# Performance work log

Hardware: AMD Instinct MI355X
Metric: run time of the kernel (lower is better)

## Reference

```python
import jax, jax.numpy as jnp
import numpy as np

B, S, E, H = 256, 512, 128, 256


def setup_inputs() -> dict:
    key = jax.random.key(0)
    ks = jax.random.split(key, 20)
    s = lambda *sh: 1.0 / np.sqrt(sh[-1])
    inp = jax.random.uniform(ks[0], (B, S, 2), dtype=jnp.float32)
    W_emb = jax.random.normal(ks[1], (E, 2), jnp.float32) * 0.5
    dec_input = jax.random.normal(ks[2], (E,), jnp.float32) * 0.1
    # encoder LSTM (input E -> hidden H), pytorch gate order i,f,g,o
    enc_Wih = jax.random.normal(ks[3], (4 * H, E), jnp.float32) * s(E)
    enc_Whh = jax.random.normal(ks[4], (4 * H, H), jnp.float32) * s(H)
    enc_bih = jnp.zeros((4 * H,), jnp.float32)
    enc_bhh = jnp.zeros((4 * H,), jnp.float32)
    # process block LSTM (input E -> hidden H)
    pb_Wih = jax.random.normal(ks[5], (4 * H, E), jnp.float32) * s(E)
    pb_Whh = jax.random.normal(ks[6], (4 * H, H), jnp.float32) * s(H)
    pb_bih = jnp.zeros((4 * H,), jnp.float32)
    pb_bhh = jnp.zeros((4 * H,), jnp.float32)
    # attention: W_q Linear(H,H), W_ref Conv1d(H,H,1), v vector
    Wq = jax.random.normal(ks[7], (H, H), jnp.float32) * s(H)
    bq = jnp.zeros((H,), jnp.float32)
    Wref = jax.random.normal(ks[8], (H, H), jnp.float32) * s(H)
    bref = jnp.zeros((H,), jnp.float32)
    V = jax.random.normal(ks[9], (H,), jnp.float32) * s(H)
    # decoder: Linear(H,H,bias=False) -> ReLU -> Linear(H,1,bias=False)
    Wd1 = jax.random.normal(ks[10], (H, H), jnp.float32) * s(H)
    Wd2 = jax.random.normal(ks[11], (1, H), jnp.float32) * s(H)
    return dict(inp=inp, W_emb=W_emb, dec_input=dec_input,
                enc_Wih=enc_Wih, enc_Whh=enc_Whh, enc_bih=enc_bih, enc_bhh=enc_bhh,
                pb_Wih=pb_Wih, pb_Whh=pb_Whh, pb_bih=pb_bih, pb_bhh=pb_bhh,
                Wq=Wq, bq=bq, Wref=Wref, bref=bref, V=V, Wd1=Wd1, Wd2=Wd2)


def _lstm_step(Whh):
    def step(carry, x_proj):
        h, c = carry
        g = x_proj + h @ Whh.T  # [B,4H]
        i, f, gg, o = jnp.split(g, 4, axis=-1)
        c = jax.nn.sigmoid(f) * c + jax.nn.sigmoid(i) * jnp.tanh(gg)
        h = jax.nn.sigmoid(o) * jnp.tanh(c)
        return (h, c), h
    return step


def reference(inp, W_emb, dec_input,
              enc_Wih, enc_Whh, enc_bih, enc_bhh,
              pb_Wih, pb_Whh, pb_bih, pb_bhh,
              Wq, bq, Wref, bref, V, Wd1, Wd2):
    b, seq, _ = inp.shape
    hdim = enc_Whh.shape[1]
    emb = inp @ W_emb.T  # [B,S,E]

    # ---- encoder LSTM over the sequence ----
    x_proj = emb @ enc_Wih.T + enc_bih + enc_bhh  # [B,S,4H]
    h0 = jnp.zeros((b, hdim), inp.dtype)
    c0 = jnp.zeros((b, hdim), inp.dtype)
    (h, c), hs = jax.lax.scan(_lstm_step(enc_Whh), (h0, c0),
                              jnp.swapaxes(x_proj, 0, 1))
    enc_out = jnp.swapaxes(hs, 0, 1)  # [B,S,H]

    # ---- process block: seq steps of single-step LSTM with constant input ----
    xp = dec_input @ pb_Wih.T + pb_bih + pb_bhh  # [4H]
    xp = jnp.broadcast_to(xp, (b, xp.shape[0]))
    step = _lstm_step(pb_Whh)
    (h, c), _ = jax.lax.scan(lambda carry, _: (step(carry, xp)[0], None),
                             (h, c), None, length=seq)

    # ---- attention (glimpse) with final hidden; inner iter loop is idempotent ----
    ref = enc_out @ Wref.T + bref            # [B,S,H]  (Conv1d kernel=1)
    q = h @ Wq.T + bq                        # [B,H]
    u = jnp.tanh(ref + q[:, None, :]) @ V    # [B,S]
    align = jax.nn.softmax(u, axis=-1)
    g_l = jnp.einsum('bs,bsh->bh', align, enc_out)  # glimpse [B,H]

    # ---- decoder head ----
    out = (jax.nn.relu(g_l @ Wd1.T)) @ Wd2.T  # [B,1]
    return out.squeeze(-1)
```

## Files before the change

kernel.cpp:

```cpp
#include <hip/hip_runtime.h>

#define B_ 256
#define S_ 512
#define E_ 128
#define H_ 256
#define FH_ 1024
#define HROW 264

typedef __bf16 bf16x8 __attribute__((ext_vector_type(8)));
typedef float f32x4 __attribute__((ext_vector_type(4)));
typedef unsigned short u16x4 __attribute__((ext_vector_type(4)));
typedef unsigned short u16x8 __attribute__((ext_vector_type(8)));

__device__ __forceinline__ unsigned short f2bf(float f) {
  union { float f; unsigned int u; } a; a.f = f;
  unsigned int u = a.u;
  u += 0x7fffu + ((u >> 16) & 1u);
  return (unsigned short)(u >> 16);
}
__device__ __forceinline__ float bf2f(unsigned short v) {
  union { unsigned int u; float f; } a; a.u = ((unsigned int)v) << 16;
  return a.f;
}
__device__ __forceinline__ float sigm(float x) { return 1.f / (1.f + __expf(-x)); }
__device__ __forceinline__ float tanh_(float x) {
  float e = __expf(2.f * x);
  return 1.f - 2.f / (e + 1.f);
}

#define OFF_ENC    ((size_t)0)
#define OFF_WHHE   ((size_t)67108864)
#define OFF_WHHP   ((size_t)67633152)
#define OFF_WREF   ((size_t)68157440)
#define OFF_MENC   ((size_t)68288512)
#define OFF_BIASE  ((size_t)68296704)
#define OFF_XPV    ((size_t)68300800)
#define OFF_FLAGS  ((size_t)68304896)
#define OFF_HX     ((size_t)68305920)
#define OFF_HFIN   ((size_t)68568064)
#define OFF_QBUF   ((size_t)68830208)
#define OFF_UBUF   ((size_t)69092352)

__global__ void k0_prep(const float* __restrict__ eWih, const float* __restrict__ eWhh,
                        const float* __restrict__ ebih, const float* __restrict__ ebhh,
                        const float* __restrict__ pWih, const float* __restrict__ pWhh,
                        const float* __restrict__ pbih, const float* __restrict__ pbhh,
                        const float* __restrict__ W_emb, const float* __restrict__ dec_in,
                        const float* __restrict__ Wref,
                        unsigned short* __restrict__ WhhE, unsigned short* __restrict__ WhhP,
                        unsigned short* __restrict__ Wrefb,
                        float* __restrict__ Menc, float* __restrict__ biasE,
                        float* __restrict__ xpv,
                        unsigned int* __restrict__ flags, float* __restrict__ ubuf) {
  int gid = blockIdx.x * blockDim.x + threadIdx.x;
  int NT = gridDim.x * blockDim.x;
  for (int i = gid; i < FH_ * H_; i += NT) {
    WhhE[i] = f2bf(eWhh[i]);
    WhhP[i] = f2bf(pWhh[i]);
  }
  for (int i = gid; i < H_ * H_; i += NT) Wrefb[i] = f2bf(Wref[i]);
  for (int i = gid; i < B_ * S_; i += NT) ubuf[i] = 0.f;
  if (gid < 256) flags[gid] = 0u;
  if (gid < FH_) {
    int n = gid;
    float m0 = 0.f, m1 = 0.f, xs = 0.f;
    for (int e = 0; e < E_; ++e) {
      float w = eWih[n * E_ + e];
      m0 += w * W_emb[e * 2 + 0];
      m1 += w * W_emb[e * 2 + 1];
      xs += pWih[n * E_ + e] * dec_in[e];
    }
    Menc[n * 2 + 0] = m0;
    Menc[n * 2 + 1] = m1;
    biasE[n] = ebih[n] + ebhh[n];
    xpv[n] = xs + pbih[n] + pbhh[n];
  }
}

__launch_bounds__(512)
__attribute__((amdgpu_waves_per_eu(2, 2)))
__global__ void k1_lstm(const float* __restrict__ inp,
                        const unsigned short* __restrict__ WhhE,
                        const unsigned short* __restrict__ WhhP,
                        const float* __restrict__ Menc, const float* __restrict__ biasE,
                        const float* __restrict__ xpv,
                        unsigned short* __restrict__ enc_out,
                        unsigned short* __restrict__ hx,
                        unsigned int* __restrict__ flags,
                        float* __restrict__ hfin) {
  __shared__ unsigned short hbuf[16 * HROW];
  __shared__ float xin[16][2];
  const int tid = threadIdx.x;
  const int wave = tid >> 6, lane = tid & 63, quad = lane >> 4, l16 = lane & 15;
  const int blk = blockIdx.x;
  const int grp = (blk & 7) | ((blk >> 4) << 3);
  const int half = (blk >> 3) & 1;
  const int kloc = (wave << 4) | l16;
  const int kcol = half * 128 + kloc;

  for (int i = tid; i < 16 * HROW; i += 512) hbuf[i] = 0;
  if (tid < 32) xin[tid >> 1][tid & 1] = inp[((grp * 16 + (tid >> 1)) * S_ + 0) * 2 + (tid & 1)];

  float c[4] = {0.f, 0.f, 0.f, 0.f};
  float hreg[4] = {0.f, 0.f, 0.f, 0.f};
  f32x4 W00, W01, W02, W03, W04, W05, W06, W07;
  f32x4 W10, W11, W12, W13, W14, W15, W16, W17;
  f32x4 W20, W21, W22, W23, W24, W25, W26, W27;
  f32x4 W30, W31, W32, W33, W34, W35, W36, W37;
  float m0c[4], m1c[4], bc[4];
  unsigned int* myflag = flags + grp * 2 + half;
  unsigned int* pflag = flags + grp * 2 + (1 - half);
  const f32x4 z4 = {0.f, 0.f, 0.f, 0.f};
  __syncthreads();

  int t = 0;
#pragma unroll 1
  for (int phase = 0; phase < 2; ++phase) {
    const unsigned short* W = phase ? WhhP : WhhE;
#define WLOAD(g)                                                        \
    {                                                                   \
      const unsigned short* wp = W + (g * 256 + kcol) * H_ + quad * 8;  \
      W##g##0 = *(const f32x4*)(wp + 0 * 32);                           \
      W##g##1 = *(const f32x4*)(wp + 1 * 32);                           \
      W##g##2 = *(const f32x4*)(wp + 2 * 32);                           \
      W##g##3 = *(const f32x4*)(wp + 3 * 32);                           \
      W##g##4 = *(const f32x4*)(wp + 4 * 32);                           \
      W##g##5 = *(const f32x4*)(wp + 5 * 32);                           \
      W##g##6 = *(const f32x4*)(wp + 6 * 32);                           \
      W##g##7 = *(const f32x4*)(wp + 7 * 32);                           \
    }
    WLOAD(0) WLOAD(1) WLOAD(2) WLOAD(3)
#undef WLOAD
    asm volatile(""
                 : "+v"(W00), "+v"(W01), "+v"(W02), "+v"(W03),
                   "+v"(W04), "+v"(W05), "+v"(W06), "+v"(W07),
                   "+v"(W10), "+v"(W11), "+v"(W12), "+v"(W13),
                   "+v"(W14), "+v"(W15), "+v"(W16), "+v"(W17),
                   "+v"(W20), "+v"(W21), "+v"(W22), "+v"(W23),
                   "+v"(W24), "+v"(W25), "+v"(W26), "+v"(W27),
                   "+v"(W30), "+v"(W31), "+v"(W32), "+v"(W33),
                   "+v"(W34), "+v"(W35), "+v"(W36), "+v"(W37));
#pragma unroll
    for (int gg = 0; gg < 4; ++gg) {
      int n = gg * 256 + kcol;
      if (phase == 0) {
        m0c[gg] = Menc[n * 2 + 0]; m1c[gg] = Menc[n * 2 + 1]; bc[gg] = biasE[n];
      } else {
        m0c[gg] = 0.f; m1c[gg] = 0.f; bc[gg] = xpv[n];
      }
    }
#pragma unroll 1
    for (int step = 0; step < 512; ++step, ++t) {
      float xpre = 0.f;
      if (phase == 0 && tid < 32) {
        int sN = (step < 511) ? step + 1 : 511;
        xpre = inp[((grp * 16 + (tid >> 1)) * S_ + sN) * 2 + (tid & 1)];
      }
      f32x4 acc0 = z4, acc1 = z4, acc2 = z4, acc3 = z4;
#define MSTEP(kt)                                                              \
      {                                                                        \
        bf16x8 Af = *(const bf16x8*)(hbuf + l16 * HROW + kt * 32 + quad * 8);  \
        acc0 = __builtin_amdgcn_mfma_f32_16x16x32_bf16(                        \
            Af, __builtin_bit_cast(bf16x8, W0##kt), acc0, 0, 0, 0);            \
        acc1 = __builtin_amdgcn_mfma_f32_16x16x32_bf16(                        \
            Af, __builtin_bit_cast(bf16x8, W1##kt), acc1, 0, 0, 0);            \
        acc2 = __builtin_amdgcn_mfma_f32_16x16x32_bf16(                        \
            Af, __builtin_bit_cast(bf16x8, W2##kt), acc2, 0, 0, 0);            \
        acc3 = __builtin_amdgcn_mfma_f32_16x16x32_bf16(                        \
            Af, __builtin_bit_cast(bf16x8, W3##kt), acc3, 0, 0, 0);            \
      }
      MSTEP(0) MSTEP(1) MSTEP(2) MSTEP(3) MSTEP(4) MSTEP(5) MSTEP(6) MSTEP(7)
#undef MSTEP
      unsigned short hb[4];
#pragma unroll
      for (int r = 0; r < 4; ++r) {
        int bl = quad * 4 + r;
        float x0 = xin[bl][0], x1 = xin[bl][1];
        float gi = acc0[r] + x0 * m0c[0] + x1 * m1c[0] + bc[0];
        float gf = acc1[r] + x0 * m0c[1] + x1 * m1c[1] + bc[1];
        float gc = acc2[r] + x0 * m0c[2] + x1 * m1c[2] + bc[2];
        float go = acc3[r] + x0 * m0c[3] + x1 * m1c[3] + bc[3];
        float cn = sigm(gf) * c[r] + sigm(gi) * tanh_(gc);
        c[r] = cn;
        hreg[r] = sigm(go) * tanh_(cn);
        hb[r] = f2bf(hreg[r]);
      }
      if (phase == 0) {
#pragma unroll
        for (int r = 0; r < 4; ++r)
          enc_out[(((size_t)(grp * 16 + quad * 4 + r) * S_ + step)) * H_ + kcol] = hb[r];
      }
      {
        unsigned short* hxs = hx + ((size_t)((t & 1) * 32 + grp * 2 + half)) * 2048;
        unsigned long long pack = (unsigned long long)hb[0] |
                                  ((unsigned long long)hb[1] << 16) |
                                  ((unsigned long long)hb[2] << 32) |
                                  ((unsigned long long)hb[3] << 48);
        __hip_atomic_store((unsigned long long*)(hxs + kloc * 16 + quad * 4), pack,
                           __ATOMIC_RELAXED, __HIP_MEMORY_SCOPE_AGENT);
      }
      __syncthreads();
      if (phase == 0 && tid < 32) xin[tid >> 1][tid & 1] = xpre;
      if (tid == 0) {
        __hip_atomic_store(myflag, (unsigned int)(t + 1), __ATOMIC_RELAXED,
                           __HIP_MEMORY_SCOPE_AGENT);
        while (__hip_atomic_load(pflag, __ATOMIC_RELAXED, __HIP_MEMORY_SCOPE_AGENT) <
               (unsigned int)(t + 1)) {
          __builtin_amdgcn_s_sleep(1);
        }
      }
      __syncthreads();
#pragma unroll
      for (int r = 0; r < 4; ++r) hbuf[(quad * 4 + r) * HROW + kcol] = hb[r];
      {
        const unsigned short* ph = hx + ((size_t)((t & 1) * 32 + grp * 2 + (1 - half))) * 2048;
        unsigned long long pv = __hip_atomic_load(
            (const unsigned long long*)(ph + tid * 4), __ATOMIC_RELAXED,
            __HIP_MEMORY_SCOPE_AGENT);
        int kp = tid >> 2, r0 = (tid & 3) * 4;
        unsigned short* dst = hbuf + (1 - half) * 128 + kp;
        dst[(size_t)(r0 + 0) * HROW] = (unsigned short)(pv);
        dst[(size_t)(r0 + 1) * HROW] = (unsigned short)(pv >> 16);
        dst[(size_t)(r0 + 2) * HROW] = (unsigned short)(pv >> 32);
        dst[(size_t)(r0 + 3) * HROW] = (unsigned short)(pv >> 48);
      }
      __syncthreads();
    }
  }
#pragma unroll
  for (int r = 0; r < 4; ++r)
    hfin[(grp * 16 + quad * 4 + r) * H_ + kcol] = hreg[r];
}

__global__ void k1b_q(const float* __restrict__ hfin, const float* __restrict__ Wq,
                      const float* __restrict__ bq, float* __restrict__ qbuf) {
  __shared__ float hl[H_];
  int b = blockIdx.x, j = threadIdx.x;
  hl[j] = hfin[b * H_ + j];
  __syncthreads();
  float s = bq[j];
  const float* w = Wq + j * H_;
  for (int k = 0; k < H_; ++k) s += hl[k] * w[k];
  qbuf[b * H_ + j] = s;
}

__launch_bounds__(512)
__global__ void k2_att(const unsigned short* __restrict__ enc_out,
                       const unsigned short* __restrict__ Wrefb,
                       const float* __restrict__ qbuf, const float* __restrict__ bref,
                       const float* __restrict__ V, float* __restrict__ ubuf) {
  __shared__ unsigned short Bs[128 * HROW];
  __shared__ float qs[128], Vs[128];
  int tid = threadIdx.x;
  int wave = tid >> 6, lane = tid & 63, quad = lane >> 4, l16 = lane & 15;
  int rowblk = blockIdx.x >> 1, nb = blockIdx.x & 1;
  int b = rowblk >> 2;
  {
    int nl = tid >> 2, seg = tid & 3;
    const unsigned short* src = Wrefb + (nb * 128 + nl) * H_ + seg * 64;
    unsigned short* dst = Bs + nl * HROW + seg * 64;
#pragma unroll
    for (int i = 0; i < 8; ++i) *(u16x8*)(dst + i * 8) = *(const u16x8*)(src + i * 8);
  }
  if (tid < 128) {
    int j = nb * 128 + tid;
    qs[tid] = qbuf[b * H_ + j] + bref[j];
    Vs[tid] = V[j];
  }
  __syncthreads();
  int rw = rowblk * 128 + wave * 16 + l16;
  const f32x4 z4 = {0.f, 0.f, 0.f, 0.f};
  f32x4 acc[8];
#pragma unroll
  for (int kt = 0; kt < 8; ++kt) {
    bf16x8 af = *(const bf16x8*)(enc_out + (size_t)rw * H_ + kt * 32 + quad * 8);
#pragma unroll
    for (int nt = 0; nt < 8; ++nt) {
      bf16x8 bfr = *(const bf16x8*)(Bs + (nt * 16 + l16) * HROW + kt * 32 + quad * 8);
      acc[nt] = __builtin_amdgcn_mfma_f32_16x16x32_bf16(af, bfr, (kt == 0) ? z4 : acc[nt],
                                                        0, 0, 0);
    }
  }
  float part[4] = {0.f, 0.f, 0.f, 0.f};
#pragma unroll
  for (int nt = 0; nt < 8; ++nt) {
    float qv = qs[nt * 16 + l16], vv = Vs[nt * 16 + l16];
#pragma unroll
    for (int r = 0; r < 4; ++r) part[r] += tanh_(acc[nt][r] + qv) * vv;
  }
#pragma unroll
  for (int m = 1; m < 16; m <<= 1) {
#pragma unroll
    for (int r = 0; r < 4; ++r) part[r] += __shfl_xor(part[r], m, 64);
  }
  if (l16 == 0) {
    int s0 = (rowblk & 3) * 128 + wave * 16 + quad * 4;
#pragma unroll
    for (int r = 0; r < 4; ++r) atomicAdd(&ubuf[b * S_ + s0 + r], part[r]);
  }
}

__global__ void k3_head(const float* __restrict__ ubuf,
                        const unsigned short* __restrict__ enc_out,
                        const float* __restrict__ Wd1, const float* __restrict__ Wd2,
                        float* __restrict__ out) {
  __shared__ float sm[512];
  __shared__ float red[256];
  __shared__ float gl[256];
  int b = blockIdx.x, tid = threadIdx.x;
  float u0 = ubuf[b * S_ + tid], u1 = ubuf[b * S_ + 256 + tid];
  red[tid] = fmaxf(u0, u1);
  __syncthreads();
  for (int s = 128; s > 0; s >>= 1) {
    if (tid < s) red[tid] = fmaxf(red[tid], red[tid + s]);
    __syncthreads();
  }
  float mx = red[0];
  __syncthreads();
  float e0 = __expf(u0 - mx), e1 = __expf(u1 - mx);
  red[tid] = e0 + e1;
  __syncthreads();
  for (int s = 128; s > 0; s >>= 1) {
    if (tid < s) red[tid] += red[tid + s];
    __syncthreads();
  }
  float inv = 1.f / red[0];
  sm[tid] = e0 * inv;
  sm[256 + tid] = e1 * inv;
  __syncthreads();
  float g = 0.f;
  const unsigned short* eo = enc_out + (size_t)b * S_ * H_ + tid;
  for (int s = 0; s < S_; ++s) g += sm[s] * bf2f(eo[(size_t)s * H_]);
  gl[tid] = g;
  __syncthreads();
  float y = 0.f;
  const float* w = Wd1 + tid * H_;
  for (int j = 0; j < H_; ++j) y += w[j] * gl[j];
  y = fmaxf(y, 0.f) * Wd2[tid];
  red[tid] = y;
  __syncthreads();
  for (int s = 128; s > 0; s >>= 1) {
    if (tid < s) red[tid] += red[tid + s];
    __syncthreads();
  }
  if (tid == 0) out[b] = red[0];
}

extern "C" void kernel_launch(void* const* d_in, const int* in_sizes, int n_in,
                              void* d_out, int out_size, void* d_ws, size_t ws_size,
                              hipStream_t stream) {
  (void)in_sizes; (void)n_in; (void)out_size; (void)ws_size;
  const float* inp    = (const float*)d_in[0];
  const float* W_emb  = (const float*)d_in[1];
  const float* dec_in = (const float*)d_in[2];
  const float* eWih   = (const float*)d_in[3];
  const float* eWhh   = (const float*)d_in[4];
  const float* ebih   = (const float*)d_in[5];
  const float* ebhh   = (const float*)d_in[6];
  const float* pWih   = (const float*)d_in[7];
  const float* pWhh   = (const float*)d_in[8];
  const float* pbih   = (const float*)d_in[9];
  const float* pbhh   = (const float*)d_in[10];
  const float* Wq     = (const float*)d_in[11];
  const float* bq     = (const float*)d_in[12];
  const float* Wref   = (const float*)d_in[13];
  const float* bref   = (const float*)d_in[14];
  const float* V      = (const float*)d_in[15];
  const float* Wd1    = (const float*)d_in[16];
  const float* Wd2    = (const float*)d_in[17];
  float* out = (float*)d_out;

  char* ws = (char*)d_ws;
  unsigned short* enc_out = (unsigned short*)(ws + OFF_ENC);
  unsigned short* WhhE    = (unsigned short*)(ws + OFF_WHHE);
  unsigned short* WhhP    = (unsigned short*)(ws + OFF_WHHP);
  unsigned short* Wrefb   = (unsigned short*)(ws + OFF_WREF);
  float* Menc  = (float*)(ws + OFF_MENC);
  float* biasE = (float*)(ws + OFF_BIASE);
  float* xpv   = (float*)(ws + OFF_XPV);
  unsigned int* flags = (unsigned int*)(ws + OFF_FLAGS);
  unsigned short* hx  = (unsigned short*)(ws + OFF_HX);
  float* hfin = (float*)(ws + OFF_HFIN);
  float* qbuf = (float*)(ws + OFF_QBUF);
  float* ubuf = (float*)(ws + OFF_UBUF);

  hipLaunchKernelGGL(k0_prep, dim3(256), dim3(256), 0, stream,
                     eWih, eWhh, ebih, ebhh, pWih, pWhh, pbih, pbhh, W_emb, dec_in,
                     Wref, WhhE, WhhP, Wrefb, Menc, biasE, xpv, flags, ubuf);
  hipLaunchKernelGGL(k1_lstm, dim3(32), dim3(512), 0, stream,
                     inp, WhhE, WhhP, Menc, biasE, xpv, enc_out, hx, flags, hfin);
  hipLaunchKernelGGL(k1b_q, dim3(256), dim3(256), 0, stream, hfin, Wq, bq, qbuf);
  hipLaunchKernelGGL(k2_att, dim3(2048), dim3(512), 0, stream,
                     enc_out, Wrefb, qbuf, bref, V, ubuf);
  hipLaunchKernelGGL(k3_head, dim3(256), dim3(256), 0, stream,
                     ubuf, enc_out, Wd1, Wd2, out);
}
```

Before: 3.224 ms.

## Overlap partner-half hidden exchange with own-half MFMA in LSTM recurrence

Splits each step's recurrent matmul into an own-half K slice, computed from local hidden state, and a partner-half slice that waits on the partner block's data. Double-buffered shared hbuf/xin and per-wave flags written right after each wave's store remove one block barrier and let the cross-block handshake overlap the first half of the MFMAs. Flags now start at 1 and hx is zeroed in prep so step 0 sees a zero partner state. This puts more polling traffic on per-wave flags and relies on relaxed atomics plus an explicit vmcnt wait for ordering.

```diff
diff --git a/kernel.cpp b/kernel.cpp
--- a/kernel.cpp
+++ b/kernel.cpp
@@ -11,6 +11,7 @@
 typedef float f32x4 __attribute__((ext_vector_type(4)));
 typedef unsigned short u16x4 __attribute__((ext_vector_type(4)));
 typedef unsigned short u16x8 __attribute__((ext_vector_type(8)));
+typedef unsigned long long u64_;
 
 __device__ __forceinline__ unsigned short f2bf(float f) {
   union { float f; unsigned int u; } a; a.f = f;
@@ -51,7 +52,8 @@
                         unsigned short* __restrict__ Wrefb,
                         float* __restrict__ Menc, float* __restrict__ biasE,
                         float* __restrict__ xpv,
-                        unsigned int* __restrict__ flags, float* __restrict__ ubuf) {
+                        unsigned int* __restrict__ flags, float* __restrict__ ubuf,
+                        unsigned short* __restrict__ hx) {
   int gid = blockIdx.x * blockDim.x + threadIdx.x;
   int NT = gridDim.x * blockDim.x;
   for (int i = gid; i < FH_ * H_; i += NT) {
@@ -60,7 +62,8 @@
   }
   for (int i = gid; i < H_ * H_; i += NT) Wrefb[i] = f2bf(Wref[i]);
   for (int i = gid; i < B_ * S_; i += NT) ubuf[i] = 0.f;
-  if (gid < 256) flags[gid] = 0u;
+  for (int i = gid; i < 131072; i += NT) hx[i] = 0;
+  if (gid < 256) flags[gid] = 1u;
   if (gid < FH_) {
     int n = gid;
     float m0 = 0.f, m1 = 0.f, xs = 0.f;
@@ -88,8 +91,8 @@
                         unsigned short* __restrict__ hx,
                         unsigned int* __restrict__ flags,
                         float* __restrict__ hfin) {
-  __shared__ unsigned short hbuf[16 * HROW];
-  __shared__ float xin[16][2];
+  __shared__ unsigned short hbuf[2][16 * HROW];
+  __shared__ float xin[2][16][2];
   const int tid = threadIdx.x;
   const int wave = tid >> 6, lane = tid & 63, quad = lane >> 4, l16 = lane & 15;
   const int blk = blockIdx.x;
@@ -97,19 +100,22 @@
   const int half = (blk >> 3) & 1;
   const int kloc = (wave << 4) | l16;
   const int kcol = half * 128 + kloc;
-
-  for (int i = tid; i < 16 * HROW; i += 512) hbuf[i] = 0;
-  if (tid < 32) xin[tid >> 1][tid & 1] = inp[((grp * 16 + (tid >> 1)) * S_ + 0) * 2 + (tid & 1)];
+  const int okt = half * 128;
+  const int pkt = 128 - okt;
+
+  for (int i = tid; i < 2 * 16 * HROW; i += 512) hbuf[0][i] = 0;
+  if (tid < 32)
+    xin[0][tid >> 1][tid & 1] = inp[((grp * 16 + (tid >> 1)) * S_ + 0) * 2 + (tid & 1)];
 
   float c[4] = {0.f, 0.f, 0.f, 0.f};
   float hreg[4] = {0.f, 0.f, 0.f, 0.f};
-  f32x4 W00, W01, W02, W03, W04, W05, W06, W07;
-  f32x4 W10, W11, W12, W13, W14, W15, W16, W17;
-  f32x4 W20, W21, W22, W23, W24, W25, W26, W27;
-  f32x4 W30, W31, W32, W33, W34, W35, W36, W37;
+  f32x4 O00, O01, O02, O03, O10, O11, O12, O13;
+  f32x4 O20, O21, O22, O23, O30, O31, O32, O33;
+  f32x4 P00, P01, P02, P03, P10, P11, P12, P13;
+  f32x4 P20, P21, P22, P23, P30, P31, P32, P33;
   float m0c[4], m1c[4], bc[4];
-  unsigned int* myflag = flags + grp * 2 + half;
-  unsigned int* pflag = flags + grp * 2 + (1 - half);
+  unsigned int* myflagw = flags + (grp * 2 + half) * 8 + wave;
+  unsigned int* pflagw = flags + (grp * 2 + (1 - half)) * 8 + wave;
   const f32x4 z4 = {0.f, 0.f, 0.f, 0.f};
   __syncthreads();
 
@@ -119,27 +125,27 @@
     const unsigned short* W = phase ? WhhP : WhhE;
 #define WLOAD(g)                                                        \
     {                                                                   \
-      const unsigned short* wp = W + (g * 256 + kcol) * H_ + quad * 8;  \
-      W##g##0 = *(const f32x4*)(wp + 0 * 32);                           \
-      W##g##1 = *(const f32x4*)(wp + 1 * 32);                           \
-      W##g##2 = *(const f32x4*)(wp + 2 * 32);                           \
-      W##g##3 = *(const f32x4*)(wp + 3 * 32);                           \
-      W##g##4 = *(const f32x4*)(wp + 4 * 32);                           \
-      W##g##5 = *(const f32x4*)(wp + 5 * 32);                           \
-      W##g##6 = *(const f32x4*)(wp + 6 * 32);                           \
-      W##g##7 = *(const f32x4*)(wp + 7 * 32);                           \
+      const unsigned short* wp = W + ((g) * 256 + kcol) * H_ + quad * 8; \
+      O##g##0 = *(const f32x4*)(wp + okt + 0);                          \
+      O##g##1 = *(const f32x4*)(wp + okt + 32);                         \
+      O##g##2 = *(const f32x4*)(wp + okt + 64);                         \
+      O##g##3 = *(const f32x4*)(wp + okt + 96);                         \
+      P##g##0 = *(const f32x4*)(wp + pkt + 0);                          \
+      P##g##1 = *(const f32x4*)(wp + pkt + 32);                         \
+      P##g##2 = *(const f32x4*)(wp + pkt + 64);                         \
+      P##g##3 = *(const f32x4*)(wp + pkt + 96);                         \
     }
     WLOAD(0) WLOAD(1) WLOAD(2) WLOAD(3)
 #undef WLOAD
     asm volatile(""
-                 : "+v"(W00), "+v"(W01), "+v"(W02), "+v"(W03),
-                   "+v"(W04), "+v"(W05), "+v"(W06), "+v"(W07),
-                   "+v"(W10), "+v"(W11), "+v"(W12), "+v"(W13),
-                   "+v"(W14), "+v"(W15), "+v"(W16), "+v"(W17),
-                   "+v"(W20), "+v"(W21), "+v"(W22), "+v"(W23),
-                   "+v"(W24), "+v"(W25), "+v"(W26), "+v"(W27),
-                   "+v"(W30), "+v"(W31), "+v"(W32), "+v"(W33),
-                   "+v"(W34), "+v"(W35), "+v"(W36), "+v"(W37));
+                 : "+v"(O00), "+v"(O01), "+v"(O02), "+v"(O03),
+                   "+v"(O10), "+v"(O11), "+v"(O12), "+v"(O13),
+                   "+v"(O20), "+v"(O21), "+v"(O22), "+v"(O23),
+                   "+v"(O30), "+v"(O31), "+v"(O32), "+v"(O33),
+                   "+v"(P00), "+v"(P01), "+v"(P02), "+v"(P03),
+                   "+v"(P10), "+v"(P11), "+v"(P12), "+v"(P13),
+                   "+v"(P20), "+v"(P21), "+v"(P22), "+v"(P23),
+                   "+v"(P30), "+v"(P31), "+v"(P32), "+v"(P33));
 #pragma unroll
     for (int gg = 0; gg < 4; ++gg) {
       int n = gg * 256 + kcol;
@@ -151,31 +157,65 @@
     }
 #pragma unroll 1
     for (int step = 0; step < 512; ++step, ++t) {
+      const int cur = t & 1, nxt = cur ^ 1;
+      const unsigned short* hbc = &hbuf[cur][0];
       float xpre = 0.f;
       if (phase == 0 && tid < 32) {
         int sN = (step < 511) ? step + 1 : 511;
         xpre = inp[((grp * 16 + (tid >> 1)) * S_ + sN) * 2 + (tid & 1)];
       }
       f32x4 acc0 = z4, acc1 = z4, acc2 = z4, acc3 = z4;
-#define MSTEP(kt)                                                              \
-      {                                                                        \
-        bf16x8 Af = *(const bf16x8*)(hbuf + l16 * HROW + kt * 32 + quad * 8);  \
-        acc0 = __builtin_amdgcn_mfma_f32_16x16x32_bf16(                        \
-            Af, __builtin_bit_cast(bf16x8, W0##kt), acc0, 0, 0, 0);            \
-        acc1 = __builtin_amdgcn_mfma_f32_16x16x32_bf16(                        \
-            Af, __builtin_bit_cast(bf16x8, W1##kt), acc1, 0, 0, 0);            \
-        acc2 = __builtin_amdgcn_mfma_f32_16x16x32_bf16(                        \
-            Af, __builtin_bit_cast(bf16x8, W2##kt), acc2, 0, 0, 0);            \
-        acc3 = __builtin_amdgcn_mfma_f32_16x16x32_bf16(                        \
-            Af, __builtin_bit_cast(bf16x8, W3##kt), acc3, 0, 0, 0);            \
-      }
-      MSTEP(0) MSTEP(1) MSTEP(2) MSTEP(3) MSTEP(4) MSTEP(5) MSTEP(6) MSTEP(7)
-#undef MSTEP
+#define MO(j)                                                                      \
+      {                                                                            \
+        bf16x8 Af = *(const bf16x8*)(hbc + l16 * HROW + okt + (j) * 32 + quad * 8);\
+        acc0 = __builtin_amdgcn_mfma_f32_16x16x32_bf16(                            \
+            Af, __builtin_bit_cast(bf16x8, O0##j), acc0, 0, 0, 0);                 \
+        acc1 = __builtin_amdgcn_mfma_f32_16x16x32_bf16(                            \
+            Af, __builtin_bit_cast(bf16x8, O1##j), acc1, 0, 0, 0);                 \
+        acc2 = __builtin_amdgcn_mfma_f32_16x16x32_bf16(                            \
+            Af, __builtin_bit_cast(bf16x8, O2##j), acc2, 0, 0, 0);                 \
+        acc3 = __builtin_amdgcn_mfma_f32_16x16x32_bf16(                            \
+            Af, __builtin_bit_cast(bf16x8, O3##j), acc3, 0, 0, 0);                 \
+      }
+      MO(0) MO(1) MO(2) MO(3)
+#undef MO
+      {
+        const unsigned int target = (unsigned int)(t + 1);
+        while (__hip_atomic_load(pflagw, __ATOMIC_RELAXED, __HIP_MEMORY_SCOPE_AGENT) <
+               target) {
+          __builtin_amdgcn_s_sleep(1);
+        }
+        const unsigned short* ph =
+            hx + ((size_t)(cur * 32 + grp * 2 + (1 - half))) * 2048;
+        u64_ pv = __hip_atomic_load((const u64_*)(ph + tid * 4), __ATOMIC_RELAXED,
+                                    __HIP_MEMORY_SCOPE_AGENT);
+        int kp = tid >> 2, r0 = (tid & 3) * 4;
+        unsigned short* dst = &hbuf[cur][0] + (1 - half) * 128 + kp;
+        dst[(size_t)(r0 + 0) * HROW] = (unsigned short)(pv);
+        dst[(size_t)(r0 + 1) * HROW] = (unsigned short)(pv >> 16);
+        dst[(size_t)(r0 + 2) * HROW] = (unsigned short)(pv >> 32);
+        dst[(size_t)(r0 + 3) * HROW] = (unsigned short)(pv >> 48);
+      }
+      __syncthreads();
+#define MP(j)                                                                      \
+      {                                                                            \
+        bf16x8 Af = *(const bf16x8*)(hbc + l16 * HROW + pkt + (j) * 32 + quad * 8);\
+        acc0 = __builtin_amdgcn_mfma_f32_16x16x32_bf16(                            \
+            Af, __builtin_bit_cast(bf16x8, P0##j), acc0, 0, 0, 0);                 \
+        acc1 = __builtin_amdgcn_mfma_f32_16x16x32_bf16(                            \
+            Af, __builtin_bit_cast(bf16x8, P1##j), acc1, 0, 0, 0);                 \
+        acc2 = __builtin_amdgcn_mfma_f32_16x16x32_bf16(                            \
+            Af, __builtin_bit_cast(bf16x8, P2##j), acc2, 0, 0, 0);                 \
+        acc3 = __builtin_amdgcn_mfma_f32_16x16x32_bf16(                            \
+            Af, __builtin_bit_cast(bf16x8, P3##j), acc3, 0, 0, 0);                 \
+      }
+      MP(0) MP(1) MP(2) MP(3)
+#undef MP
       unsigned short hb[4];
 #pragma unroll
       for (int r = 0; r < 4; ++r) {
         int bl = quad * 4 + r;
-        float x0 = xin[bl][0], x1 = xin[bl][1];
+        float x0 = xin[cur][bl][0], x1 = xin[cur][bl][1];
         float gi = acc0[r] + x0 * m0c[0] + x1 * m1c[0] + bc[0];
         float gf = acc1[r] + x0 * m0c[1] + x1 * m1c[1] + bc[1];
         float gc = acc2[r] + x0 * m0c[2] + x1 * m1c[2] + bc[2];
@@ -185,45 +225,25 @@
         hreg[r] = sigm(go) * tanh_(cn);
         hb[r] = f2bf(hreg[r]);
       }
+      {
+        unsigned short* hxs = hx + ((size_t)(nxt * 32 + grp * 2 + half)) * 2048;
+        u64_ pack = (u64_)hb[0] | ((u64_)hb[1] << 16) | ((u64_)hb[2] << 32) |
+                    ((u64_)hb[3] << 48);
+        __hip_atomic_store((u64_*)(hxs + kloc * 16 + quad * 4), pack,
+                           __ATOMIC_RELAXED, __HIP_MEMORY_SCOPE_AGENT);
+      }
+      asm volatile("s_waitcnt vmcnt(0)");
+      if (lane == 0)
+        __hip_atomic_store(myflagw, (unsigned int)(t + 2), __ATOMIC_RELAXED,
+                           __HIP_MEMORY_SCOPE_AGENT);
       if (phase == 0) {
 #pragma unroll
         for (int r = 0; r < 4; ++r)
           enc_out[(((size_t)(grp * 16 + quad * 4 + r) * S_ + step)) * H_ + kcol] = hb[r];
       }
-      {
-        unsigned short* hxs = hx + ((size_t)((t & 1) * 32 + grp * 2 + half)) * 2048;
-        unsigned long long pack = (unsigned long long)hb[0] |
-                                  ((unsigned long long)hb[1] << 16) |
-                                  ((unsigned long long)hb[2] << 32) |
-                                  ((unsigned long long)hb[3] << 48);
-        __hip_atomic_store((unsigned long long*)(hxs + kloc * 16 + quad * 4), pack,
-                           __ATOMIC_RELAXED, __HIP_MEMORY_SCOPE_AGENT);
-      }
-      __syncthreads();
-      if (phase == 0 && tid < 32) xin[tid >> 1][tid & 1] = xpre;
-      if (tid == 0) {
-        __hip_atomic_store(myflag, (unsigned int)(t + 1), __ATOMIC_RELAXED,
-                           __HIP_MEMORY_SCOPE_AGENT);
-        while (__hip_atomic_load(pflag, __ATOMIC_RELAXED, __HIP_MEMORY_SCOPE_AGENT) <
-               (unsigned int)(t + 1)) {
-          __builtin_amdgcn_s_sleep(1);
-        }
-      }
-      __syncthreads();
-#pragma unroll
-      for (int r = 0; r < 4; ++r) hbuf[(quad * 4 + r) * HROW + kcol] = hb[r];
-      {
-        const unsigned short* ph = hx + ((size_t)((t & 1) * 32 + grp * 2 + (1 - half))) * 2048;
-        unsigned long long pv = __hip_atomic_load(
-            (const unsigned long long*)(ph + tid * 4), __ATOMIC_RELAXED,
-            __HIP_MEMORY_SCOPE_AGENT);
-        int kp = tid >> 2, r0 = (tid & 3) * 4;
-        unsigned short* dst = hbuf + (1 - half) * 128 + kp;
-        dst[(size_t)(r0 + 0) * HROW] = (unsigned short)(pv);
-        dst[(size_t)(r0 + 1) * HROW] = (unsigned short)(pv >> 16);
-        dst[(size_t)(r0 + 2) * HROW] = (unsigned short)(pv >> 32);
-        dst[(size_t)(r0 + 3) * HROW] = (unsigned short)(pv >> 48);
-      }
+#pragma unroll
+      for (int r = 0; r < 4; ++r) hbuf[nxt][(quad * 4 + r) * HROW + kcol] = hb[r];
+      if (phase == 0 && tid < 32) xin[nxt][tid >> 1][tid & 1] = xpre;
       __syncthreads();
     }
   }
@@ -386,7 +406,7 @@
 
   hipLaunchKernelGGL(k0_prep, dim3(256), dim3(256), 0, stream,
                      eWih, eWhh, ebih, ebhh, pWih, pWhh, pbih, pbhh, W_emb, dec_in,
-                     Wref, WhhE, WhhP, Wrefb, Menc, biasE, xpv, flags, ubuf);
+                     Wref, WhhE, WhhP, Wrefb, Menc, biasE, xpv, flags, ubuf, hx);
   hipLaunchKernelGGL(k1_lstm, dim3(32), dim3(512), 0, stream,
                      inp, WhhE, WhhP, Menc, biasE, xpv, enc_out, hx, flags, hfin);
   hipLaunchKernelGGL(k1b_q, dim3(256), dim3(256), 0, stream, hfin, Wq, bq, qbuf);
```

After: 3.369 ms. 1.04x slower.

## Process two batch groups per LSTM block with double-buffered state and per-wave flags

Applied to the files above, without the earlier changes.

Each persistent LSTM block now runs the recurrence for two 16-row batch groups instead of one, so the grid shrinks from 32 to 16 blocks. The shared hidden-state and input buffers are double-buffered, which drops one of the two block-wide barriers per step. The cross-block handshake becomes a per-wave flag: each wave waits only on its partner wave's slice of the exchanged hidden state. This halves the number of synchronizing blocks and gives each wave two independent GEMM chains to interleave. In exchange, each step does twice the serial work per block, and the flag array now needs eight times as many entries, which must be zeroed and sized correctly.

```diff
diff --git a/kernel.cpp b/kernel.cpp
--- a/kernel.cpp
+++ b/kernel.cpp
@@ -11,6 +11,7 @@
 typedef float f32x4 __attribute__((ext_vector_type(4)));
 typedef unsigned short u16x4 __attribute__((ext_vector_type(4)));
 typedef unsigned short u16x8 __attribute__((ext_vector_type(8)));
+typedef unsigned long long u64_;
 
 __device__ __forceinline__ unsigned short f2bf(float f) {
   union { float f; unsigned int u; } a; a.f = f;
@@ -88,28 +89,37 @@
                         unsigned short* __restrict__ hx,
                         unsigned int* __restrict__ flags,
                         float* __restrict__ hfin) {
-  __shared__ unsigned short hbuf[16 * HROW];
-  __shared__ float xin[16][2];
+  __shared__ unsigned short hbA[2][16 * HROW];
+  __shared__ unsigned short hbB[2][16 * HROW];
+  __shared__ float xinA[2][16][2], xinB[2][16][2];
   const int tid = threadIdx.x;
   const int wave = tid >> 6, lane = tid & 63, quad = lane >> 4, l16 = lane & 15;
   const int blk = blockIdx.x;
-  const int grp = (blk & 7) | ((blk >> 4) << 3);
-  const int half = (blk >> 3) & 1;
+  const int p = blk & 7;
+  const int half = blk >> 3;
+  const int gA = p * 2, gB = p * 2 + 1;
   const int kloc = (wave << 4) | l16;
   const int kcol = half * 128 + kloc;
 
-  for (int i = tid; i < 16 * HROW; i += 512) hbuf[i] = 0;
-  if (tid < 32) xin[tid >> 1][tid & 1] = inp[((grp * 16 + (tid >> 1)) * S_ + 0) * 2 + (tid & 1)];
-
-  float c[4] = {0.f, 0.f, 0.f, 0.f};
-  float hreg[4] = {0.f, 0.f, 0.f, 0.f};
+  for (int i = tid; i < 16 * HROW; i += 512) {
+    hbA[0][i] = 0; hbB[0][i] = 0;
+  }
+  if (tid < 64) {
+    int g_ = tid >> 5, tt = tid & 31;
+    int grp = g_ ? gB : gA;
+    float v = inp[((grp * 16 + (tt >> 1)) * S_ + 0) * 2 + (tt & 1)];
+    if (g_) xinB[0][tt >> 1][tt & 1] = v; else xinA[0][tt >> 1][tt & 1] = v;
+  }
+
+  float cA[4] = {0.f, 0.f, 0.f, 0.f}, cB[4] = {0.f, 0.f, 0.f, 0.f};
+  float hrA[4] = {0.f, 0.f, 0.f, 0.f}, hrB[4] = {0.f, 0.f, 0.f, 0.f};
   f32x4 W00, W01, W02, W03, W04, W05, W06, W07;
   f32x4 W10, W11, W12, W13, W14, W15, W16, W17;
   f32x4 W20, W21, W22, W23, W24, W25, W26, W27;
   f32x4 W30, W31, W32, W33, W34, W35, W36, W37;
   float m0c[4], m1c[4], bc[4];
-  unsigned int* myflag = flags + grp * 2 + half;
-  unsigned int* pflag = flags + grp * 2 + (1 - half);
+  unsigned int* myflag = flags + ((p * 2 + half) << 3) + wave;
+  unsigned int* pflag = flags + ((p * 2 + (1 - half)) << 3) + wave;
   const f32x4 z4 = {0.f, 0.f, 0.f, 0.f};
   __syncthreads();
 
@@ -119,7 +129,7 @@
     const unsigned short* W = phase ? WhhP : WhhE;
 #define WLOAD(g)                                                        \
     {                                                                   \
-      const unsigned short* wp = W + (g * 256 + kcol) * H_ + quad * 8;  \
+      const unsigned short* wp = W + ((g) * 256 + kcol) * H_ + quad * 8; \
       W##g##0 = *(const f32x4*)(wp + 0 * 32);                           \
       W##g##1 = *(const f32x4*)(wp + 1 * 32);                           \
       W##g##2 = *(const f32x4*)(wp + 2 * 32);                           \
@@ -149,87 +159,136 @@
         m0c[gg] = 0.f; m1c[gg] = 0.f; bc[gg] = xpv[n];
       }
     }
+
+#define MS(kt, HB)                                                             \
+    {                                                                          \
+      bf16x8 Af = *(const bf16x8*)((HB) + l16 * HROW + kt * 32 + quad * 8);    \
+      acc0 = __builtin_amdgcn_mfma_f32_16x16x32_bf16(                          \
+          Af, __builtin_bit_cast(bf16x8, W0##kt), acc0, 0, 0, 0);              \
+      acc1 = __builtin_amdgcn_mfma_f32_16x16x32_bf16(                          \
+          Af, __builtin_bit_cast(bf16x8, W1##kt), acc1, 0, 0, 0);              \
+      acc2 = __builtin_amdgcn_mfma_f32_16x16x32_bf16(                          \
+          Af, __builtin_bit_cast(bf16x8, W2##kt), acc2, 0, 0, 0);              \
+      acc3 = __builtin_amdgcn_mfma_f32_16x16x32_bf16(                          \
+          Af, __builtin_bit_cast(bf16x8, W3##kt), acc3, 0, 0, 0);              \
+    }
+#define GEMM8(HB) MS(0, HB) MS(1, HB) MS(2, HB) MS(3, HB) \
+                  MS(4, HB) MS(5, HB) MS(6, HB) MS(7, HB)
+
 #pragma unroll 1
     for (int step = 0; step < 512; ++step, ++t) {
+      const int cur = t & 1, nxt = cur ^ 1;
       float xpre = 0.f;
-      if (phase == 0 && tid < 32) {
+      if (phase == 0 && tid < 64) {
+        int g_ = tid >> 5, tt = tid & 31;
+        int grp = g_ ? gB : gA;
         int sN = (step < 511) ? step + 1 : 511;
-        xpre = inp[((grp * 16 + (tid >> 1)) * S_ + sN) * 2 + (tid & 1)];
-      }
-      f32x4 acc0 = z4, acc1 = z4, acc2 = z4, acc3 = z4;
-#define MSTEP(kt)                                                              \
-      {                                                                        \
-        bf16x8 Af = *(const bf16x8*)(hbuf + l16 * HROW + kt * 32 + quad * 8);  \
-        acc0 = __builtin_amdgcn_mfma_f32_16x16x32_bf16(                        \
-            Af, __builtin_bit_cast(bf16x8, W0##kt), acc0, 0, 0, 0);            \
-        acc1 = __builtin_amdgcn_mfma_f32_16x16x32_bf16(                        \
-            Af, __builtin_bit_cast(bf16x8, W1##kt), acc1, 0, 0, 0);            \
-        acc2 = __builtin_amdgcn_mfma_f32_16x16x32_bf16(                        \
-            Af, __builtin_bit_cast(bf16x8, W2##kt), acc2, 0, 0, 0);            \
-        acc3 = __builtin_amdgcn_mfma_f32_16x16x32_bf16(                        \
-            Af, __builtin_bit_cast(bf16x8, W3##kt), acc3, 0, 0, 0);            \
-      }
-      MSTEP(0) MSTEP(1) MSTEP(2) MSTEP(3) MSTEP(4) MSTEP(5) MSTEP(6) MSTEP(7)
-#undef MSTEP
-      unsigned short hb[4];
-#pragma unroll
-      for (int r = 0; r < 4; ++r) {
-        int bl = quad * 4 + r;
-        float x0 = xin[bl][0], x1 = xin[bl][1];
-        float gi = acc0[r] + x0 * m0c[0] + x1 * m1c[0] + bc[0];
-        float gf = acc1[r] + x0 * m0c[1] + x1 * m1c[1] + bc[1];
-        float gc = acc2[r] + x0 * m0c[2] + x1 * m1c[2] + bc[2];
-        float go = acc3[r] + x0 * m0c[3] + x1 * m1c[3] + bc[3];
-        float cn = sigm(gf) * c[r] + sigm(gi) * tanh_(gc);
-        c[r] = cn;
-        hreg[r] = sigm(go) * tanh_(cn);
-        hb[r] = f2bf(hreg[r]);
-      }
-      if (phase == 0) {
-#pragma unroll
-        for (int r = 0; r < 4; ++r)
-          enc_out[(((size_t)(grp * 16 + quad * 4 + r) * S_ + step)) * H_ + kcol] = hb[r];
-      }
+        xpre = inp[((grp * 16 + (tt >> 1)) * S_ + sN) * 2 + (tt & 1)];
+      }
+      unsigned short hb4A[4], hb4B[4];
       {
-        unsigned short* hxs = hx + ((size_t)((t & 1) * 32 + grp * 2 + half)) * 2048;
-        unsigned long long pack = (unsigned long long)hb[0] |
-                                  ((unsigned long long)hb[1] << 16) |
-                                  ((unsigned long long)hb[2] << 32) |
-                                  ((unsigned long long)hb[3] << 48);
-        __hip_atomic_store((unsigned long long*)(hxs + kloc * 16 + quad * 4), pack,
+        f32x4 acc0 = z4, acc1 = z4, acc2 = z4, acc3 = z4;
+        GEMM8(&hbA[cur][0])
+#pragma unroll
+        for (int r = 0; r < 4; ++r) {
+          int bl = quad * 4 + r;
+          float x0 = xinA[cur][bl][0], x1 = xinA[cur][bl][1];
+          float gi = acc0[r] + x0 * m0c[0] + x1 * m1c[0] + bc[0];
+          float gf = acc1[r] + x0 * m0c[1] + x1 * m1c[1] + bc[1];
+          float gc = acc2[r] + x0 * m0c[2] + x1 * m1c[2] + bc[2];
+          float go = acc3[r] + x0 * m0c[3] + x1 * m1c[3] + bc[3];
+          float cn = sigm(gf) * cA[r] + sigm(gi) * tanh_(gc);
+          cA[r] = cn;
+          hrA[r] = sigm(go) * tanh_(cn);
+          hb4A[r] = f2bf(hrA[r]);
+        }
+        if (phase == 0) {
+#pragma unroll
+          for (int r = 0; r < 4; ++r)
+            enc_out[(((size_t)(gA * 16 + quad * 4 + r) * S_ + step)) * H_ + kcol] = hb4A[r];
+        }
+        unsigned short* hxs = hx + ((size_t)(nxt * 32 + gA * 2 + half)) * 2048;
+        u64_ pack = (u64_)hb4A[0] | ((u64_)hb4A[1] << 16) | ((u64_)hb4A[2] << 32) |
+                    ((u64_)hb4A[3] << 48);
+        __hip_atomic_store((u64_*)(hxs + kloc * 16 + quad * 4), pack,
                            __ATOMIC_RELAXED, __HIP_MEMORY_SCOPE_AGENT);
-      }
-      __syncthreads();
-      if (phase == 0 && tid < 32) xin[tid >> 1][tid & 1] = xpre;
-      if (tid == 0) {
-        __hip_atomic_store(myflag, (unsigned int)(t + 1), __ATOMIC_RELAXED,
+#pragma unroll
+        for (int r = 0; r < 4; ++r) hbA[nxt][(quad * 4 + r) * HROW + kcol] = hb4A[r];
+      }
+      {
+        f32x4 acc0 = z4, acc1 = z4, acc2 = z4, acc3 = z4;
+        GEMM8(&hbB[cur][0])
+#pragma unroll
+        for (int r = 0; r < 4; ++r) {
+          int bl = quad * 4 + r;
+          float x0 = xinB[cur][bl][0], x1 = xinB[cur][bl][1];
+          float gi = acc0[r] + x0 * m0c[0] + x1 * m1c[0] + bc[0];
+          float gf = acc1[r] + x0 * m0c[1] + x1 * m1c[1] + bc[1];
+          float gc = acc2[r] + x0 * m0c[2] + x1 * m1c[2] + bc[2];
+          float go = acc3[r] + x0 * m0c[3] + x1 * m1c[3] + bc[3];
+          float cn = sigm(gf) * cB[r] + sigm(gi) * tanh_(gc);
+          cB[r] = cn;
+          hrB[r] = sigm(go) * tanh_(cn);
+          hb4B[r] = f2bf(hrB[r]);
+        }
+        if (phase == 0) {
+#pragma unroll
+          for (int r = 0; r < 4; ++r)
+            enc_out[(((size_t)(gB * 16 + quad * 4 + r) * S_ + step)) * H_ + kcol] = hb4B[r];
+        }
+        unsigned short* hxs = hx + ((size_t)(nxt * 32 + gB * 2 + half)) * 2048;
+        u64_ pack = (u64_)hb4B[0] | ((u64_)hb4B[1] << 16) | ((u64_)hb4B[2] << 32) |
+                    ((u64_)hb4B[3] << 48);
+        __hip_atomic_store((u64_*)(hxs + kloc * 16 + quad * 4), pack,
+                           __ATOMIC_RELAXED, __HIP_MEMORY_SCOPE_AGENT);
+#pragma unroll
+        for (int r = 0; r < 4; ++r) hbB[nxt][(quad * 4 + r) * HROW + kcol] = hb4B[r];
+      }
+      asm volatile("s_waitcnt vmcnt(0)" ::: "memory");
+      if (lane == 0)
+        __hip_atomic_store(myflag, (unsigned int)(t + 2), __ATOMIC_RELAXED,
                            __HIP_MEMORY_SCOPE_AGENT);
+      if (phase == 0 && tid < 64) {
+        int g_ = tid >> 5, tt = tid & 31;
+        if (g_) xinB[nxt][tt >> 1][tt & 1] = xpre;
+        else xinA[nxt][tt >> 1][tt & 1] = xpre;
+      }
+      {
+        const unsigned int target = (unsigned int)(t + 2);
         while (__hip_atomic_load(pflag, __ATOMIC_RELAXED, __HIP_MEMORY_SCOPE_AGENT) <
-               (unsigned int)(t + 1)) {
+               target) {
           __builtin_amdgcn_s_sleep(1);
         }
+        const unsigned short* phA =
+            hx + ((size_t)(nxt * 32 + gA * 2 + (1 - half))) * 2048;
+        const unsigned short* phB =
+            hx + ((size_t)(nxt * 32 + gB * 2 + (1 - half))) * 2048;
+        u64_ pvA = __hip_atomic_load((const u64_*)(phA + tid * 4), __ATOMIC_RELAXED,
+                                     __HIP_MEMORY_SCOPE_AGENT);
+        u64_ pvB = __hip_atomic_load((const u64_*)(phB + tid * 4), __ATOMIC_RELAXED,
+                                     __HIP_MEMORY_SCOPE_AGENT);
+        int kp = tid >> 2, r0 = (tid & 3) * 4;
+        unsigned short* dA = &hbA[nxt][0] + (1 - half) * 128 + kp;
+        dA[(size_t)(r0 + 0) * HROW] = (unsigned short)(pvA);
+        dA[(size_t)(r0 + 1) * HROW] = (unsigned short)(pvA >> 16);
+        dA[(size_t)(r0 + 2) * HROW] = (unsigned short)(pvA >> 32);
+        dA[(size_t)(r0 + 3) * HROW] = (unsigned short)(pvA >> 48);
+        unsigned short* dB = &hbB[nxt][0] + (1 - half) * 128 + kp;
+        dB[(size_t)(r0 + 0) * HROW] = (unsigned short)(pvB);
+        dB[(size_t)(r0 + 1) * HROW] = (unsigned short)(pvB >> 16);
+        dB[(size_t)(r0 + 2) * HROW] = (unsigned short)(pvB >> 32);
+        dB[(size_t)(r0 + 3) * HROW] = (unsigned short)(pvB >> 48);
       }
       __syncthreads();
-#pragma unroll
-      for (int r = 0; r < 4; ++r) hbuf[(quad * 4 + r) * HROW + kcol] = hb[r];
-      {
-        const unsigned short* ph = hx + ((size_t)((t & 1) * 32 + grp * 2 + (1 - half))) * 2048;
-        unsigned long long pv = __hip_atomic_load(
-            (const unsigned long long*)(ph + tid * 4), __ATOMIC_RELAXED,
-            __HIP_MEMORY_SCOPE_AGENT);
-        int kp = tid >> 2, r0 = (tid & 3) * 4;
-        unsigned short* dst = hbuf + (1 - half) * 128 + kp;
-        dst[(size_t)(r0 + 0) * HROW] = (unsigned short)(pv);
-        dst[(size_t)(r0 + 1) * HROW] = (unsigned short)(pv >> 16);
-        dst[(size_t)(r0 + 2) * HROW] = (unsigned short)(pv >> 32);
-        dst[(size_t)(r0 + 3) * HROW] = (unsigned short)(pv >> 48);
-      }
-      __syncthreads();
-    }
-  }
-#pragma unroll
-  for (int r = 0; r < 4; ++r)
-    hfin[(grp * 16 + quad * 4 + r) * H_ + kcol] = hreg[r];
+    }
+#undef GEMM8
+#undef MS
+  }
+#pragma unroll
+  for (int r = 0; r < 4; ++r) {
+    hfin[(gA * 16 + quad * 4 + r) * H_ + kcol] = hrA[r];
+    hfin[(gB * 16 + quad * 4 + r) * H_ + kcol] = hrB[r];
+  }
 }
 
 __global__ void k1b_q(const float* __restrict__ hfin, const float* __restrict__ Wq,
@@ -387,7 +446,7 @@
   hipLaunchKernelGGL(k0_prep, dim3(256), dim3(256), 0, stream,
                      eWih, eWhh, ebih, ebhh, pWih, pWhh, pbih, pbhh, W_emb, dec_in,
                      Wref, WhhE, WhhP, Wrefb, Menc, biasE, xpv, flags, ubuf);
-  hipLaunchKernelGGL(k1_lstm, dim3(32), dim3(512), 0, stream,
+  hipLaunchKernelGGL(k1_lstm, dim3(16), dim3(512), 0, stream,
                      inp, WhhE, WhhP, Menc, biasE, xpv, enc_out, hx, flags, hfin);
   hipLaunchKernelGGL(k1b_q, dim3(256), dim3(256), 0, stream, hfin, Wq, bq, qbuf);
   hipLaunchKernelGGL(k2_att, dim3(2048), dim3(512), 0, stream,
```

Result: slower. 6.256 ms (+94.0%).
